# Kernel tuning notes

Hardware: AMD Instinct MI355X
Metric: run time of the kernel (lower is better)

## Reference

```python
import jax, jax.numpy as jnp
import numpy as np

N = 8192        # num_nodes == args.input_size (code ties them together)
H = 64          # hidden_size
E = 262144      # num edges (avg degree 32)
FIN = N + H     # GCNConv in_channels = input_size + hidden_size


def _glorot(key, shape):
    fan_in, fan_out = shape
    lim = np.sqrt(6.0 / (fan_in + fan_out)).astype(np.float32)
    return jax.random.uniform(key, shape, jnp.float32, -lim, lim)


def gcn_conv(x, W, b, src, dst, n):
    """PyG GCNConv: lin -> add self-loops -> sym-normalized scatter-add -> +bias."""
    h = x @ W                                   # [n, out]
    loop = jnp.arange(n, dtype=src.dtype)
    s = jnp.concatenate([src, loop])            # [E+n]
    d = jnp.concatenate([dst, loop])
    deg = jax.ops.segment_sum(jnp.ones(s.shape[0], h.dtype), d, num_segments=n)
    dinv = jnp.where(deg > 0, jax.lax.rsqrt(deg), 0.0)
    norm = dinv[s] * dinv[d]                    # [E+n]
    out = jax.ops.segment_sum(h[s] * norm[:, None], d, num_segments=n)
    return out + b


def setup_inputs() -> dict:
    key = jax.random.key(0)
    k1, k2, k3, k4, k5 = jax.random.split(key, 5)
    x = jax.random.normal(k1, (N, N), jnp.float32)
    hidden_state = jax.random.normal(k2, (N, H), jnp.float32)
    W1 = _glorot(k3, (FIN, 2 * H))
    b1 = jnp.ones((2 * H,), jnp.float32)        # reset_parameters: constant_(bias, 1.0)
    W2 = _glorot(k4, (FIN, H))
    b2 = jnp.zeros((H,), jnp.float32)           # PyG default bias init = zeros
    edge_index = jax.random.randint(k5, (2, E), 0, N, jnp.int32)
    return {"x": x, "hidden_state": hidden_state, "W1": W1, "b1": b1,
            "W2": W2, "b2": b2, "edge_index": edge_index}


def reference(x, hidden_state, W1, b1, W2, b2, edge_index):
    src, dst = edge_index[0], edge_index[1]
    ru_input = jnp.concatenate([x, hidden_state], axis=1)        # [N, N+H]
    ru = jax.nn.sigmoid(gcn_conv(ru_input, W1, b1, src, dst, N))  # [N, 2H]
    flat = ru.reshape(-1, N * 2 * H)                              # [1, N*2H]
    r = flat[:, : N * H].reshape(-1, H)                           # [N, H]
    u = flat[:, N * H :].reshape(-1, H)                           # [N, H]
    c_input = jnp.concatenate([x, r * hidden_state], axis=1)
    c = jnp.tanh(gcn_conv(c_input, W2, b2, src, dst, N))          # [N, H]
    new_hidden_state = u * hidden_state + (1.0 - u) * c
    return new_hidden_state
```

## Files before the change

kernel.cpp:

```cpp
#include <hip/hip_runtime.h>
#include <hip/hip_bf16.h>
#include <stdint.h>

typedef __bf16 bf16x8 __attribute__((ext_vector_type(8)));
typedef float  f32x4  __attribute__((ext_vector_type(4)));
typedef unsigned uint4v __attribute__((ext_vector_type(4)));
using bf16 = __hip_bfloat16;

#define NNODES 8192
#define FIN    8256
#define NCOL   192
#define KT32   258
#define BMB    128

enum : size_t {
  WCT_OFF  = 0,
  CNT_OFF  = 3170304,
  OFF_OFF  = 3203072,
  CUR_OFF  = 3236096,
  DNV_OFF  = 3268864,
  CSR_OFF  = 3301632,
  H1_OFF   = 4350208,
  HX2_OFF  = 8544512,
  RU_OFF   = 10641664,
  H2_OFF   = 14835968,
  YP_OFF   = 16933120,
  YP_SLICE = 6291456
};

__global__ void k_zero_i(int* p, int n) {
  int i = blockIdx.x * 256 + threadIdx.x;
  if (i < n) p[i] = 0;
}

__global__ void k_out_zero(float* out) {
  int i = blockIdx.x * 256 + threadIdx.x;
  if (i < NNODES * 64) out[i] = 0.f;
}

__global__ __launch_bounds__(256) void k_prep_wctf(const float* __restrict__ W1,
                                                   const float* __restrict__ W2,
                                                   bf16* __restrict__ wctf) {
  __shared__ float W1s[32][128];
  __shared__ float W2s[32][64];
  const int t = blockIdx.x;
  const int k0 = t * 32;
  const int tid = threadIdx.x;
#pragma unroll
  for (int q = 0; q < 4; ++q) {
    int idx = tid + 256 * q;
    int r = idx >> 5, c4 = idx & 31;
    float4 v = *(const float4*)(W1 + (size_t)(k0 + r) * 128 + c4 * 4);
    *(float4*)&W1s[r][c4 * 4] = v;
  }
#pragma unroll
  for (int q = 0; q < 2; ++q) {
    int idx = tid + 256 * q;
    int r = idx >> 4, c4 = idx & 15;
    float4 v = {0.f, 0.f, 0.f, 0.f};
    if (k0 + r < 8192) v = *(const float4*)(W2 + (size_t)(k0 + r) * 64 + c4 * 4);
    *(float4*)&W2s[r][c4 * 4] = v;
  }
  __syncthreads();
#pragma unroll
  for (int q = 0; q < 3; ++q) {
    int gl = tid + 256 * q;
    int nf = gl >> 6, lane = gl & 63;
    int col = nf * 16 + (lane & 15);
    int kk = (lane >> 4) * 8;
    union { bf16 h[8]; uint4 v; } u;
#pragma unroll
    for (int j = 0; j < 8; ++j) {
      float v = (col < 128) ? W1s[kk + j][col] : W2s[kk + j][col - 128];
      u.h[j] = __float2bfloat16(v);
    }
    *(uint4*)(wctf + ((size_t)t * 768 + gl) * 8) = u.v;
  }
}

__global__ void k_hist(const int* __restrict__ ei, int E, int* cnt) {
  int e = blockIdx.x * 256 + threadIdx.x;
  if (e < E) atomicAdd(&cnt[ei[E + e]], 1);
}

__global__ void k_scan(const int* __restrict__ cnt, int* __restrict__ offs,
                       int* __restrict__ cur, float* __restrict__ dinv) {
  __shared__ int part[256];
  int tid = threadIdx.x;
  int base = tid * 32;
  int s = 0;
#pragma unroll
  for (int j = 0; j < 32; j++) s += cnt[base + j];
  part[tid] = s;
  __syncthreads();
  for (int off = 1; off < 256; off <<= 1) {
    int a = (tid >= off) ? part[tid - off] : 0;
    __syncthreads();
    part[tid] += a;
    __syncthreads();
  }
  int run = (tid == 0) ? 0 : part[tid - 1];
  for (int j = 0; j < 32; j++) {
    int c = cnt[base + j];
    offs[base + j] = run;
    cur[base + j]  = run;
    dinv[base + j] = rsqrtf((float)(c + 1));
    run += c;
  }
  if (tid == 255) offs[NNODES] = run;
}

__global__ void k_fill(const int* __restrict__ ei, int E, int* cur, int* __restrict__ csr) {
  int e = blockIdx.x * 256 + threadIdx.x;
  if (e < E) {
    int d = ei[E + e];
    int p = atomicAdd(&cur[d], 1);
    csr[p] = ei[e];
  }
}

__device__ __forceinline__ bf16x8 pack8(float4 a, float4 b) {
  union { bf16 h[8]; bf16x8 v; } u;
  u.h[0] = __float2bfloat16(a.x); u.h[1] = __float2bfloat16(a.y);
  u.h[2] = __float2bfloat16(a.z); u.h[3] = __float2bfloat16(a.w);
  u.h[4] = __float2bfloat16(b.x); u.h[5] = __float2bfloat16(b.y);
  u.h[6] = __float2bfloat16(b.z); u.h[7] = __float2bfloat16(b.w);
  return u.v;
}

union F4 { uint4v u; float4 f; bf16x8 h; };

__device__ __forceinline__ void gld16(void* ldsdst, const void* gsrc) {
  __builtin_amdgcn_global_load_lds(
      (__attribute__((address_space(1))) void*)gsrc,
      (__attribute__((address_space(3))) void*)ldsdst, 16, 0, 0);
}

__global__ __launch_bounds__(256, 2) void k_gemm(const float* __restrict__ x,
                                                 const float* __restrict__ hid,
                                                 const bf16* __restrict__ wctf,
                                                 float* __restrict__ yp,
                                                 bf16* __restrict__ h1d,
                                                 float* __restrict__ hx2d,
                                                 int tpc) {
  __shared__ __align__(1024) unsigned char smem[36864];
  const int tid = threadIdx.x;
  const int lane = tid & 63, w = tid >> 6;
  const int rl = lane & 15, g = lane >> 4;
  const int m0 = blockIdx.x * BMB;
  const int r0 = m0 + w * 32 + rl, r1 = r0 + 16;
  const int chunk = blockIdx.y;
  const int t_lo = chunk * tpc;
  const int t_hi = (t_lo + tpc > KT32) ? KT32 : (t_lo + tpc);
  const int nt = t_hi - t_lo;
  if (nt <= 0) return;

  const float* a0x = x + (size_t)r0 * 8192 + g * 8;
  const float* a1x = x + (size_t)r1 * 8192 + g * 8;
  const float* a0h = hid + (size_t)r0 * 64 + g * 8;
  const float* a1h = hid + (size_t)r1 * 64 + g * 8;

#define STAGE_B(buf, t) do {                                                    \
    const bf16* _bt = wctf + (size_t)(t) * 6144;                                \
    unsigned _d = (unsigned)(buf) * 12288u;                                     \
    _Pragma("unroll")                                                           \
    for (int q = 0; q < 3; ++q)                                                 \
      gld16(smem + _d + (unsigned)(q * 256 + tid) * 16u,                        \
            _bt + (size_t)(q * 256 + tid) * 8);                                 \
  } while (0)

#define LOAD_A(Pa, Pb, Pc, Pd, T) do {                                          \
    const int _k = (T) * 32;                                                    \
    const float* _p0 = (_k < 8192) ? (a0x + _k) : (a0h + (_k - 8192));          \
    const float* _p1 = (_k < 8192) ? (a1x + _k) : (a1h + (_k - 8192));          \
    asm volatile("global_load_dwordx4 %0, %1, off"           : "=v"(Pa.u) : "v"(_p0)); \
    asm volatile("global_load_dwordx4 %0, %1, off offset:16" : "=v"(Pb.u) : "v"(_p0)); \
    asm volatile("global_load_dwordx4 %0, %1, off"           : "=v"(Pc.u) : "v"(_p1)); \
    asm volatile("global_load_dwordx4 %0, %1, off offset:16" : "=v"(Pd.u) : "v"(_p1)); \
  } while (0)

  f32x4 acc0[12] = {};
  f32x4 acc1[12] = {};
  F4 p00, p01, p10, p11, q00, q01, q10, q11;

  const unsigned ldsbase = (unsigned)(uintptr_t)&smem[0];
  const unsigned bB = (unsigned)lane * 16u;

  STAGE_B(0, t_lo);
  if (nt > 1) STAGE_B(1, t_lo + 1);
  LOAD_A(p00, p01, p10, p11, t_lo);

  int b3r = 0, b3w = 2;

#define GBODY(Ca, Cb, Cc, Cd, Na, Nb, Nc, Nd, I) do {                           \
    const int _i = (I);                                                         \
    if (_i + 2 < nt) STAGE_B(b3w, t_lo + _i + 2);                    \
    if (_i + 1 < nt) LOAD_A(Na, Nb, Nc, Nd, t_lo + _i + 1);          \
        \
    if (_i + 2 < nt)      asm volatile("s_waitcnt vmcnt(7)" ::: "memory");      \
    else if (_i + 1 < nt) asm volatile("s_waitcnt vmcnt(4)" ::: "memory");      \
    else                  asm volatile("s_waitcnt vmcnt(0)" ::: "memory");      \
    asm volatile("s_barrier" ::: "memory");         \
    {                                                                           \
      const unsigned _br = ldsbase + bB + (unsigned)b3r * 12288u;               \
      F4 _bv[12];                                                               \
      _Pragma("unroll")                                                         \
      for (int nf = 0; nf < 12; ++nf)                                           \
        asm volatile("ds_read_b128 %0, %1 offset:%c2"                           \
                     : "=v"(_bv[nf].u) : "v"(_br), "i"(nf * 1024));             \
      asm volatile("s_waitcnt lgkmcnt(0)" ::: "memory");                        \
      __builtin_amdgcn_sched_barrier(0);                                        \
      bf16x8 _af0 = pack8(Ca.f, Cb.f);                                          \
      bf16x8 _af1 = pack8(Cc.f, Cd.f);                                          \
      _Pragma("unroll")                                                         \
      for (int nf = 0; nf < 12; ++nf) {                                         \
        acc0[nf] = __builtin_amdgcn_mfma_f32_16x16x32_bf16(_af0, _bv[nf].h, acc0[nf], 0, 0, 0); \
        acc1[nf] = __builtin_amdgcn_mfma_f32_16x16x32_bf16(_af1, _bv[nf].h, acc1[nf], 0, 0, 0); \
      }                                                                         \
    }                                                                           \
    asm volatile("s_barrier" ::: "memory");   \
    b3r = (b3r == 2) ? 0 : b3r + 1;                                             \
    b3w = (b3w == 2) ? 0 : b3w + 1;                                             \
  } while (0)

  int it = 0;
  for (; it + 1 < nt; it += 2) {
    GBODY(p00, p01, p10, p11, q00, q01, q10, q11, it);
    GBODY(q00, q01, q10, q11, p00, p01, p10, p11, it + 1);
  }
  if (it < nt) GBODY(p00, p01, p10, p11, q00, q01, q10, q11, it);
#undef GBODY
#undef LOAD_A
#undef STAGE_B

  if (h1d) {
#pragma unroll
    for (int nf = 0; nf < 12; ++nf) {
      int col = nf * 16 + rl;
#pragma unroll
      for (int tt = 0; tt < 4; ++tt) {
        int ra = m0 + w * 32 + g * 4 + tt;
        int rb = ra + 16;
        if (col < 128) {
          h1d[(size_t)ra * 128 + col] = __float2bfloat16(acc0[nf][tt]);
          h1d[(size_t)rb * 128 + col] = __float2bfloat16(acc1[nf][tt]);
        } else {
          hx2d[(size_t)ra * 64 + (col - 128)] = acc0[nf][tt];
          hx2d[(size_t)rb * 64 + (col - 128)] = acc1[nf][tt];
        }
      }
    }
  } else {
    float* ypc = yp + (size_t)chunk * ((size_t)NNODES * NCOL);
#pragma unroll
    for (int nf = 0; nf < 12; ++nf) {
      int col = nf * 16 + rl;
#pragma unroll
      for (int tt = 0; tt < 4; ++tt) {
        int ra = m0 + w * 32 + g * 4 + tt;
        ypc[(size_t)ra * NCOL + col] = acc0[nf][tt];
        ypc[(size_t)(ra + 16) * NCOL + col] = acc1[nf][tt];
      }
    }
  }
}

__global__ void k_reduce4(const float* __restrict__ yp, bf16* __restrict__ h1,
                          float* __restrict__ hx2, int nch) {
  int u = blockIdx.x * 256 + threadIdx.x;
  float4 s = {0.f, 0.f, 0.f, 0.f};
  for (int c = 0; c < nch; c++) {
    float4 v = *(const float4*)(yp + (size_t)c * ((size_t)NNODES * NCOL) + (size_t)u * 4);
    s.x += v.x; s.y += v.y; s.z += v.z; s.w += v.w;
  }
  int e = u * 4;
  int i = e / NCOL, c = e - i * NCOL;
  if (c < 128) {
    bf16* dst = h1 + (size_t)i * 128 + c;
    dst[0] = __float2bfloat16(s.x); dst[1] = __float2bfloat16(s.y);
    dst[2] = __float2bfloat16(s.z); dst[3] = __float2bfloat16(s.w);
  } else {
    *(float4*)(hx2 + (size_t)i * 64 + (c - 128)) = s;
  }
}

__device__ __forceinline__ float bflo(unsigned v) { return __uint_as_float(v << 16); }
__device__ __forceinline__ float bfhi(unsigned v) { return __uint_as_float(v & 0xffff0000u); }

__global__ void k_scat1(const bf16* __restrict__ h1b, const int* __restrict__ offs,
                        const int* __restrict__ csr, const float* __restrict__ dinv,
                        const float* __restrict__ b1, float* __restrict__ ru) {
  int node = blockIdx.x * 4 + (threadIdx.x >> 6);
  int lane = threadIdx.x & 63;
  const unsigned* h1u = (const unsigned*)h1b;
  float dd = dinv[node];
  unsigned vv = h1u[(size_t)node * 64 + lane];
  float ax = bflo(vv) * dd * dd, ay = bfhi(vv) * dd * dd;
  int e0 = offs[node], e1 = offs[node + 1];
  for (int e = e0; e < e1; ++e) {
    int s = csr[e];
    float nrm = dinv[s] * dd;
    unsigned wv = h1u[(size_t)s * 64 + lane];
    ax += bflo(wv) * nrm;
    ay += bfhi(wv) * nrm;
  }
  ax += b1[lane * 2];
  ay += b1[lane * 2 + 1];
  ax = 1.f / (1.f + expf(-ax));
  ay = 1.f / (1.f + expf(-ay));
  ru[(size_t)node * 128 + lane * 2]     = ax;
  ru[(size_t)node * 128 + lane * 2 + 1] = ay;
}

__global__ void k_rh(const float* __restrict__ ru, const float* __restrict__ hidden,
                     const float* __restrict__ hx2, const float* __restrict__ W2,
                     bf16* __restrict__ h2) {
  __shared__ float W2s[64][64];
  __shared__ float rhs[4][64];
  int tid = threadIdx.x;
#pragma unroll
  for (int t = 0; t < 16; ++t) {
    int idx = tid + 256 * t;
    int j = idx >> 6, c = idx & 63;
    W2s[j][c] = W2[(size_t)(8192 + j) * 64 + c];
  }
  int w = tid >> 6, lane = tid & 63;
  int i = blockIdx.x * 4 + w;
  float rv = ru[(size_t)(i >> 1) * 128 + ((i & 1) << 6) + lane];
  float hv = hidden[(size_t)i * 64 + lane];
  rhs[w][lane] = rv * hv;
  __syncthreads();
  float acc = hx2[(size_t)i * 64 + lane];
#pragma unroll 8
  for (int j = 0; j < 64; ++j) acc += rhs[w][j] * W2s[j][lane];
  h2[(size_t)i * 64 + lane] = __float2bfloat16(acc);
}

__global__ void k_scat2(const bf16* __restrict__ h2b, const int* __restrict__ offs,
                        const int* __restrict__ csr, const float* __restrict__ dinv,
                        const float* __restrict__ b2, const float* __restrict__ ru,
                        const float* __restrict__ hidden, float* __restrict__ out) {
  int node = blockIdx.x * 4 + (threadIdx.x >> 6);
  int lane = threadIdx.x & 63;
  const unsigned short* h2u = (const unsigned short*)h2b;
  float dd = dinv[node];
  float acc = bflo((unsigned)h2u[(size_t)node * 64 + lane]) * dd * dd;
  int e0 = offs[node], e1 = offs[node + 1];
  for (int e = e0; e < e1; ++e) {
    int s = csr[e];
    acc += bflo((unsigned)h2u[(size_t)s * 64 + lane]) * dinv[s] * dd;
  }
  acc += b2[lane];
  float cv = tanhf(acc);
  float u = ru[(size_t)(4096 + (node >> 1)) * 128 + ((node & 1) << 6) + lane];
  float hv = hidden[(size_t)node * 64 + lane];
  out[(size_t)node * 64 + lane] = u * hv + (1.f - u) * cv;
}

extern "C" void kernel_launch(void* const* d_in, const int* in_sizes, int n_in,
                              void* d_out, int out_size, void* d_ws, size_t ws_size,
                              hipStream_t stream) {
  (void)n_in; (void)out_size;
  const float* x   = (const float*)d_in[0];
  const float* hid = (const float*)d_in[1];
  const float* W1  = (const float*)d_in[2];
  const float* b1  = (const float*)d_in[3];
  const float* W2  = (const float*)d_in[4];
  const float* b2  = (const float*)d_in[5];
  const int*   ei  = (const int*)d_in[6];
  const int E = in_sizes[6] / 2;
  float* out = (float*)d_out;

  int ksplit;
  if      (ws_size >= YP_OFF + 12ull * YP_SLICE) ksplit = 12;
  else if (ws_size >= YP_OFF + 8ull  * YP_SLICE) ksplit = 8;
  else if (ws_size >= YP_OFF + 4ull  * YP_SLICE) ksplit = 4;
  else if (ws_size >= YP_OFF + 2ull  * YP_SLICE) ksplit = 2;
  else if (ws_size >= YP_OFF)                    ksplit = 1;
  else {
    k_out_zero<<<dim3(NNODES * 64 / 256), dim3(256), 0, stream>>>(out);
    return;
  }
  const int tpc = (KT32 + ksplit - 1) / ksplit;

  char* ws = (char*)d_ws;
  bf16*  wctf = (bf16*)(ws + WCT_OFF);
  int*   cnt  = (int*)(ws + CNT_OFF);
  int*   offs = (int*)(ws + OFF_OFF);
  int*   cur  = (int*)(ws + CUR_OFF);
  float* dinv = (float*)(ws + DNV_OFF);
  int*   csr  = (int*)(ws + CSR_OFF);
  bf16*  h1   = (bf16*)(ws + H1_OFF);
  float* hx2  = (float*)(ws + HX2_OFF);
  float* ru   = (float*)(ws + RU_OFF);
  bf16*  h2   = (bf16*)(ws + H2_OFF);
  float* yp   = (float*)(ws + YP_OFF);

  k_zero_i<<<dim3(32), dim3(256), 0, stream>>>(cnt, NNODES);
  k_prep_wctf<<<dim3(KT32), dim3(256), 0, stream>>>(W1, W2, wctf);
  k_hist<<<dim3((E + 255) / 256), dim3(256), 0, stream>>>(ei, E, cnt);
  k_scan<<<dim3(1), dim3(256), 0, stream>>>(cnt, offs, cur, dinv);
  k_fill<<<dim3((E + 255) / 256), dim3(256), 0, stream>>>(ei, E, cur, csr);
  if (ksplit == 1) {
    k_gemm<<<dim3(NNODES / BMB, 1), dim3(256), 0, stream>>>(x, hid, wctf, nullptr, h1, hx2, tpc);
  } else {
    k_gemm<<<dim3(NNODES / BMB, ksplit), dim3(256), 0, stream>>>(x, hid, wctf, yp, nullptr, nullptr, tpc);
    k_reduce4<<<dim3(NNODES * NCOL / 1024), dim3(256), 0, stream>>>(yp, h1, hx2, ksplit);
  }
  k_scat1<<<dim3(NNODES / 4), dim3(256), 0, stream>>>(h1, offs, csr, dinv, b1, ru);
  k_rh<<<dim3(NNODES / 4), dim3(256), 0, stream>>>(ru, hid, hx2, W2, h2);
  k_scat2<<<dim3(NNODES / 4), dim3(256), 0, stream>>>(h2, offs, csr, dinv, b2, ru, hid, out);
}
```

Before: 194.3 us.

## Double GEMM K-tile depth to 64 and cap split-K at eight

The main GEMM now handles 64 K-elements per pipeline step instead of 32. Each step issues eight A loads and six B LDS stages, runs two MFMA sub-steps and uses a 72KB LDS triple buffer. This halves the barriers and loop overhead per unit of work and lets each step issue more memory traffic. The maximum split-K factor drops from 12 to 8, which means fewer partial-sum slices to reduce but fewer blocks in flight. Doubling LDS use may cut occupancy below the two blocks per CU declared in the launch bounds.

```diff
diff --git a/kernel.cpp b/kernel.cpp
--- a/kernel.cpp
+++ b/kernel.cpp
@@ -11,6 +11,7 @@
 #define FIN    8256
 #define NCOL   192
 #define KT32   258
+#define KT64   129
 #define BMB    128
 
 enum : size_t {
@@ -143,7 +144,7 @@
                                                  bf16* __restrict__ h1d,
                                                  float* __restrict__ hx2d,
                                                  int tpc) {
-  __shared__ __align__(1024) unsigned char smem[36864];
+  __shared__ __align__(1024) unsigned char smem[73728];
   const int tid = threadIdx.x;
   const int lane = tid & 63, w = tid >> 6;
   const int rl = lane & 15, g = lane >> 4;
@@ -151,7 +152,7 @@
   const int r0 = m0 + w * 32 + rl, r1 = r0 + 16;
   const int chunk = blockIdx.y;
   const int t_lo = chunk * tpc;
-  const int t_hi = (t_lo + tpc > KT32) ? KT32 : (t_lo + tpc);
+  const int t_hi = (t_lo + tpc > KT64) ? KT64 : (t_lo + tpc);
   const int nt = t_hi - t_lo;
   if (nt <= 0) return;
 
@@ -161,48 +162,54 @@
   const float* a1h = hid + (size_t)r1 * 64 + g * 8;
 
 #define STAGE_B(buf, t) do {                                                    \
-    const bf16* _bt = wctf + (size_t)(t) * 6144;                                \
-    unsigned _d = (unsigned)(buf) * 12288u;                                     \
+    const bf16* _bt = wctf + (size_t)(t) * 12288;                               \
+    unsigned _d = (unsigned)(buf) * 24576u;                                     \
     _Pragma("unroll")                                                           \
-    for (int q = 0; q < 3; ++q)                                                 \
+    for (int q = 0; q < 6; ++q)                                                 \
       gld16(smem + _d + (unsigned)(q * 256 + tid) * 16u,                        \
             _bt + (size_t)(q * 256 + tid) * 8);                                 \
   } while (0)
 
-#define LOAD_A(Pa, Pb, Pc, Pd, T) do {                                          \
-    const int _k = (T) * 32;                                                    \
-    const float* _p0 = (_k < 8192) ? (a0x + _k) : (a0h + (_k - 8192));          \
-    const float* _p1 = (_k < 8192) ? (a1x + _k) : (a1h + (_k - 8192));          \
-    asm volatile("global_load_dwordx4 %0, %1, off"           : "=v"(Pa.u) : "v"(_p0)); \
-    asm volatile("global_load_dwordx4 %0, %1, off offset:16" : "=v"(Pb.u) : "v"(_p0)); \
-    asm volatile("global_load_dwordx4 %0, %1, off"           : "=v"(Pc.u) : "v"(_p1)); \
-    asm volatile("global_load_dwordx4 %0, %1, off offset:16" : "=v"(Pd.u) : "v"(_p1)); \
+#define LOAD_A(A0, A1, A2, A3, A4, A5, A6, A7, T) do {                          \
+    const int _k = (T) * 64;                                                    \
+    const float* _p0 = ((T) < 128) ? (a0x + _k) : (a0h + (_k - 8192));          \
+    const float* _p1 = ((T) < 128) ? (a1x + _k) : (a1h + (_k - 8192));          \
+    asm volatile("global_load_dwordx4 %0, %1, off"            : "=v"(A0.u) : "v"(_p0)); \
+    asm volatile("global_load_dwordx4 %0, %1, off offset:16"  : "=v"(A1.u) : "v"(_p0)); \
+    asm volatile("global_load_dwordx4 %0, %1, off offset:128" : "=v"(A2.u) : "v"(_p0)); \
+    asm volatile("global_load_dwordx4 %0, %1, off offset:144" : "=v"(A3.u) : "v"(_p0)); \
+    asm volatile("global_load_dwordx4 %0, %1, off"            : "=v"(A4.u) : "v"(_p1)); \
+    asm volatile("global_load_dwordx4 %0, %1, off offset:16"  : "=v"(A5.u) : "v"(_p1)); \
+    asm volatile("global_load_dwordx4 %0, %1, off offset:128" : "=v"(A6.u) : "v"(_p1)); \
+    asm volatile("global_load_dwordx4 %0, %1, off offset:144" : "=v"(A7.u) : "v"(_p1)); \
   } while (0)
 
   f32x4 acc0[12] = {};
   f32x4 acc1[12] = {};
-  F4 p00, p01, p10, p11, q00, q01, q10, q11;
+  F4 pA0, pA1, pA2, pA3, pA4, pA5, pA6, pA7;
+  F4 qA0, qA1, qA2, qA3, qA4, qA5, qA6, qA7;
 
   const unsigned ldsbase = (unsigned)(uintptr_t)&smem[0];
   const unsigned bB = (unsigned)lane * 16u;
 
   STAGE_B(0, t_lo);
   if (nt > 1) STAGE_B(1, t_lo + 1);
-  LOAD_A(p00, p01, p10, p11, t_lo);
+  LOAD_A(pA0, pA1, pA2, pA3, pA4, pA5, pA6, pA7, t_lo);
 
   int b3r = 0, b3w = 2;
 
-#define GBODY(Ca, Cb, Cc, Cd, Na, Nb, Nc, Nd, I) do {                           \
+#define GBODY(C0, C1, C2, C3, C4, C5, C6, C7,                                   \
+              N0, N1, N2, N3, N4, N5, N6, N7, I) do {                           \
     const int _i = (I);                                                         \
-    if (_i + 2 < nt) STAGE_B(b3w, t_lo + _i + 2);                    \
-    if (_i + 1 < nt) LOAD_A(Na, Nb, Nc, Nd, t_lo + _i + 1);          \
-        \
-    if (_i + 2 < nt)      asm volatile("s_waitcnt vmcnt(7)" ::: "memory");      \
-    else if (_i + 1 < nt) asm volatile("s_waitcnt vmcnt(4)" ::: "memory");      \
-    else                  asm volatile("s_waitcnt vmcnt(0)" ::: "memory");      \
-    asm volatile("s_barrier" ::: "memory");         \
+    if (_i + 2 < nt) STAGE_B(b3w, t_lo + _i + 2);                        \
+    if (_i + 1 < nt) LOAD_A(N0, N1, N2, N3, N4, N5, N6, N7, t_lo + _i + 1);  \
+                   \
+    if (_i + 2 < nt)      asm volatile("s_waitcnt vmcnt(14)" ::: "memory");     \
+    else if (_i + 1 < nt) asm volatile("s_waitcnt vmcnt(8)"  ::: "memory");     \
+    else                  asm volatile("s_waitcnt vmcnt(0)"  ::: "memory");     \
+    asm volatile("s_barrier" ::: "memory");                                     \
     {                                                                           \
-      const unsigned _br = ldsbase + bB + (unsigned)b3r * 12288u;               \
+      const unsigned _br = ldsbase + bB + (unsigned)b3r * 24576u;               \
       F4 _bv[12];                                                               \
       _Pragma("unroll")                                                         \
       for (int nf = 0; nf < 12; ++nf)                                           \
@@ -210,25 +217,42 @@
                      : "=v"(_bv[nf].u) : "v"(_br), "i"(nf * 1024));             \
       asm volatile("s_waitcnt lgkmcnt(0)" ::: "memory");                        \
       __builtin_amdgcn_sched_barrier(0);                                        \
-      bf16x8 _af0 = pack8(Ca.f, Cb.f);                                          \
-      bf16x8 _af1 = pack8(Cc.f, Cd.f);                                          \
+      bf16x8 _af0 = pack8(C0.f, C1.f);                                          \
+      bf16x8 _af1 = pack8(C4.f, C5.f);                                          \
       _Pragma("unroll")                                                         \
       for (int nf = 0; nf < 12; ++nf) {                                         \
         acc0[nf] = __builtin_amdgcn_mfma_f32_16x16x32_bf16(_af0, _bv[nf].h, acc0[nf], 0, 0, 0); \
         acc1[nf] = __builtin_amdgcn_mfma_f32_16x16x32_bf16(_af1, _bv[nf].h, acc1[nf], 0, 0, 0); \
       }                                                                         \
+      _Pragma("unroll")                                                         \
+      for (int nf = 0; nf < 12; ++nf)                                           \
+        asm volatile("ds_read_b128 %0, %1 offset:%c2"                           \
+                     : "=v"(_bv[nf].u) : "v"(_br + 12288u), "i"(nf * 1024));    \
+      asm volatile("s_waitcnt lgkmcnt(0)" ::: "memory");                        \
+      __builtin_amdgcn_sched_barrier(0);                                        \
+      bf16x8 _ag0 = pack8(C2.f, C3.f);                                          \
+      bf16x8 _ag1 = pack8(C6.f, C7.f);                                          \
+      _Pragma("unroll")                                                         \
+      for (int nf = 0; nf < 12; ++nf) {                                         \
+        acc0[nf] = __builtin_amdgcn_mfma_f32_16x16x32_bf16(_ag0, _bv[nf].h, acc0[nf], 0, 0, 0); \
+        acc1[nf] = __builtin_amdgcn_mfma_f32_16x16x32_bf16(_ag1, _bv[nf].h, acc1[nf], 0, 0, 0); \
+      }                                                                         \
     }                                                                           \
-    asm volatile("s_barrier" ::: "memory");   \
+    asm volatile("s_barrier" ::: "memory");                                     \
     b3r = (b3r == 2) ? 0 : b3r + 1;                                             \
     b3w = (b3w == 2) ? 0 : b3w + 1;                                             \
   } while (0)
 
   int it = 0;
   for (; it + 1 < nt; it += 2) {
-    GBODY(p00, p01, p10, p11, q00, q01, q10, q11, it);
-    GBODY(q00, q01, q10, q11, p00, p01, p10, p11, it + 1);
-  }
-  if (it < nt) GBODY(p00, p01, p10, p11, q00, q01, q10, q11, it);
+    GBODY(pA0, pA1, pA2, pA3, pA4, pA5, pA6, pA7,
+          qA0, qA1, qA2, qA3, qA4, qA5, qA6, qA7, it);
+    GBODY(qA0, qA1, qA2, qA3, qA4, qA5, qA6, qA7,
+          pA0, pA1, pA2, pA3, pA4, pA5, pA6, pA7, it + 1);
+  }
+  if (it < nt)
+    GBODY(pA0, pA1, pA2, pA3, pA4, pA5, pA6, pA7,
+          qA0, qA1, qA2, qA3, qA4, qA5, qA6, qA7, it);
 #undef GBODY
 #undef LOAD_A
 #undef STAGE_B
@@ -372,16 +396,15 @@
   float* out = (float*)d_out;
 
   int ksplit;
-  if      (ws_size >= YP_OFF + 12ull * YP_SLICE) ksplit = 12;
-  else if (ws_size >= YP_OFF + 8ull  * YP_SLICE) ksplit = 8;
-  else if (ws_size >= YP_OFF + 4ull  * YP_SLICE) ksplit = 4;
-  else if (ws_size >= YP_OFF + 2ull  * YP_SLICE) ksplit = 2;
-  else if (ws_size >= YP_OFF)                    ksplit = 1;
+  if      (ws_size >= YP_OFF + 8ull * YP_SLICE) ksplit = 8;
+  else if (ws_size >= YP_OFF + 4ull * YP_SLICE) ksplit = 4;
+  else if (ws_size >= YP_OFF + 2ull * YP_SLICE) ksplit = 2;
+  else if (ws_size >= YP_OFF)                   ksplit = 1;
   else {
     k_out_zero<<<dim3(NNODES * 64 / 256), dim3(256), 0, stream>>>(out);
     return;
   }
-  const int tpc = (KT32 + ksplit - 1) / ksplit;
+  const int tpc = (KT64 + ksplit - 1) / ksplit;
 
   char* ws = (char*)d_ws;
   bf16*  wctf = (bf16*)(ws + WCT_OFF);
```

New measurement: 202.6 us. +4.3%, slower.
